# Optimization experiments

Measured on AMD Instinct MI355X. Metric: run time of the kernel, lower is better.

## Reference

```python
import jax, jax.numpy as jnp
import numpy as np

THRESHOLD = 0.2
MARGIN = 2
TEMP = 0.1


def _margin_mask(h0, w0, h1, w1):
    # interior-valid mask per spatial dim (margin_remove=b removed on both ends;
    # mask0 is None so h0s=h0 etc. and the symmetric trailing-b removal applies)
    def interior(n):
        i = jnp.arange(n)
        return (i >= MARGIN) & (i < n - MARGIN)
    m = (interior(h0)[:, None, None, None]
         & interior(w0)[None, :, None, None]
         & interior(h1)[None, None, :, None]
         & interior(w1)[None, None, None, :])  # [h0,w0,h1,w1]
    return m.reshape(1, h0 * w0, h1 * w1)


def setup_inputs() -> dict:
    key = jax.random.key(0)
    k0, k1 = jax.random.split(key)
    x0 = jax.random.normal(k0, (1, 6400, 256), dtype=jnp.float32)
    x1 = jax.random.normal(k1, (1, 6400, 256), dtype=jnp.float32)
    return {"x0": x0, "x1": x1, "h0": 80, "w0": 80, "h1": 80, "w1": 80}


def reference(x0, x1, h0, w0, h1, w1):
    n, l, c = x0.shape
    s = x1.shape[1]
    # similarities = einsum / c / temp
    sim = jnp.einsum('nlc,nsc->nls', x0, x1) / (c * TEMP)
    # dual softmax confidences
    conf = jax.nn.softmax(sim, axis=2) * jax.nn.softmax(sim, axis=1)
    # threshold + margin removal (mask0=None branch of _remove_mask_margin)
    mask = (conf > THRESHOLD) & _margin_mask(h0, w0, h1, w1)
    # mutual top-1 (argmax via equality with row/col max, exactly as torch)
    m0 = conf == jnp.max(conf, axis=2, keepdims=True)
    m1 = conf == jnp.max(conf, axis=1, keepdims=True)
    mask = mask & m0 & m1
    # fixed-shape encoding of the match extraction: nonzero(mask) <=> nonzero of
    # this masked confidence map; matched confidences are its nonzero values.
    return conf * mask.astype(conf.dtype)
```

## Files before the change

### kernel.cpp

```cpp
#include <hip/hip_runtime.h>

namespace {

constexpr int Ldim = 6400;
constexpr int Sdim = 6400;
constexpr float INV_CT = 0.0390625f;
constexpr float THR = 0.2f;
constexpr int CAP = 65536;

typedef __attribute__((ext_vector_type(8))) short short8;
typedef __attribute__((ext_vector_type(4))) float f32x4;

__device__ __forceinline__ void atomicMaxPosF(float* addr, float v) {
  atomicMax(reinterpret_cast<unsigned int*>(addr), __float_as_uint(v));
}

__device__ __forceinline__ bool valid80(int idx) {
  const int i = idx / 80;
  const int j = idx - i * 80;
  return (i >= 2) & (i < 78) & (j >= 2) & (j < 78);
}

__device__ __forceinline__ unsigned short f2bf(float v) {
  unsigned u = __float_as_uint(v);
  return (unsigned short)((u + 0x7fffu + ((u >> 16) & 1u)) >> 16);
}

__device__ __forceinline__ float conf1(float s, float rs, float cs) {
  return expf(2.f * s) / (rs * cs);
}

typedef const __attribute__((address_space(1))) unsigned int guint;
typedef __attribute__((address_space(3))) unsigned int suint;
__device__ __forceinline__ void gload16(const void* g, void* l) {
  __builtin_amdgcn_global_load_lds((guint*)g, (suint*)l, 16, 0, 0);
}


__global__ __launch_bounds__(256)
void k_split2(const float* __restrict__ X0, const float* __restrict__ X1,
              unsigned short* __restrict__ XA, unsigned short* __restrict__ XB,
              float* __restrict__ stats ) {
  const int half = Ldim * 32 / 256;
  if (blockIdx.x == 2 * half) {
    for (int i = threadIdx.x; i < 4 * Ldim + 4; i += 256) stats[i] = 0.f;
    return;
  }
  const bool second = blockIdx.x >= half;
  const float* X = second ? X1 : X0;
  unsigned short* Xh = second ? XB : XA;
  const int g = (blockIdx.x - (second ? half : 0)) * 256 + threadIdx.x;
  const int r = g >> 5;
  const int gt = g & 31;
  const float* src = X + ((size_t)r << 8) + (gt << 3);
  const float4 a = *reinterpret_cast<const float4*>(src);
  const float4 b = *reinterpret_cast<const float4*>(src + 4);
  short8 hv;
  hv[0] = (short)f2bf(a.x); hv[1] = (short)f2bf(a.y);
  hv[2] = (short)f2bf(a.z); hv[3] = (short)f2bf(a.w);
  hv[4] = (short)f2bf(b.x); hv[5] = (short)f2bf(b.y);
  hv[6] = (short)f2bf(b.z); hv[7] = (short)f2bf(b.w);
  const int gp = (gt & 3) ^ ((r >> 1) & 3);
  const size_t dst = ((size_t)((gt >> 2) * Ldim + r) * 4 + gp) << 3;
  *reinterpret_cast<short8*>(Xh + dst) = hv;
}

__device__ __forceinline__ void gemm128(
    const unsigned short* __restrict__ A, const unsigned short* __restrict__ B,
    int m0, int n0, int wave, int lane,
    unsigned short (*sA)[4096], unsigned short (*sB)[4096], f32x4 acc[4][4]) {
  const int wr = wave >> 1, wc = wave & 1;
  const int ll = lane & 15;
  const int lg = lane >> 4;
  const int arow = lane >> 2;
  const int gsel = (lane & 3) * 8;

#pragma unroll
  for (int mi = 0; mi < 4; ++mi)
#pragma unroll
    for (int ni = 0; ni < 4; ++ni) acc[mi][ni] = (f32x4){0.f, 0.f, 0.f, 0.f};

  auto stage = [&](int slot, int ks) {
    const size_t kb = (size_t)ks * (Ldim * 32);
#pragma unroll
    for (int p = 0; p < 2; ++p) {
      const int ch = wave * 2 + p;
      const size_t asrc = kb + (size_t)(m0 + ch * 16 + arow) * 32 + gsel;
      const size_t bsrc = kb + (size_t)(n0 + ch * 16 + arow) * 32 + gsel;
      gload16(A + asrc, &sA[slot][ch * 512]);
      gload16(B + bsrc, &sB[slot][ch * 512]);
    }
  };

  stage(0, 0);
  __syncthreads();

  for (int ks = 0; ks < 8; ++ks) {
    const int cur = ks & 1;
    if (ks < 7) stage(cur ^ 1, ks + 1);

    auto rd = [&](unsigned short* S, int row) -> short8 {
      const int gp = lg ^ ((row >> 1) & 3);
      return *reinterpret_cast<const short8*>(&S[(row * 4 + gp) * 8]);
    };
    short8 af[4], bfv[4];
#pragma unroll
    for (int mi = 0; mi < 4; ++mi) af[mi] = rd(sA[cur], wr * 64 + mi * 16 + ll);
#pragma unroll
    for (int ni = 0; ni < 4; ++ni) bfv[ni] = rd(sB[cur], wc * 64 + ni * 16 + ll);
#pragma unroll
    for (int mi = 0; mi < 4; ++mi)
#pragma unroll
      for (int ni = 0; ni < 4; ++ni)
        acc[mi][ni] = __builtin_amdgcn_mfma_f32_16x16x32_bf16(af[mi], bfv[ni], acc[mi][ni], 0, 0, 0);

    __syncthreads();
  }

#pragma unroll
  for (int mi = 0; mi < 4; ++mi)
#pragma unroll
    for (int ni = 0; ni < 4; ++ni) acc[mi][ni] *= INV_CT;
}

__global__ __launch_bounds__(256)
void k_gemm_all(const unsigned short* __restrict__ A, const unsigned short* __restrict__ B,
                float* __restrict__ Rsum, float* __restrict__ Csum,
                unsigned int* __restrict__ cnt, unsigned int* __restrict__ cidx,
                float* __restrict__ csim, float* __restrict__ out) {
  __shared__ unsigned short sA[2][4096], sB[2][4096];
  const int tid = threadIdx.x;
  const int lane = tid & 63, wave = tid >> 6;
  const int wr = wave >> 1, wc = wave & 1;
  const int ll = lane & 15, lg = lane >> 4;
  const int bx = blockIdx.x % (Sdim / 128);
  const int by = blockIdx.x / (Sdim / 128);
  const int m0 = by * 128, n0 = bx * 128;

  f32x4 acc[4][4];
  gemm128(A, B, m0, n0, wave, lane, sA, sB, acc);

  {
    const float4 z = make_float4(0.f, 0.f, 0.f, 0.f);
#pragma unroll
    for (int i = 0; i < 16; ++i) {
      const int e = i * 256 + tid;
      const int row = e >> 5;
      const int c4 = e & 31;
      *reinterpret_cast<float4*>(&out[(size_t)(m0 + row) * Sdim + n0 + c4 * 4]) = z;
    }
  }

  float re[16];
  float colp[4] = {0.f, 0.f, 0.f, 0.f};
#pragma unroll
  for (int mi = 0; mi < 4; ++mi)
#pragma unroll
    for (int r = 0; r < 4; ++r) {
      float s = 0.f;
#pragma unroll
      for (int ni = 0; ni < 4; ++ni) {
        const float e = expf(acc[mi][ni][r]);
        s += e;
        colp[ni] += e;
      }
      s += __shfl_xor(s, 1);
      s += __shfl_xor(s, 2);
      s += __shfl_xor(s, 4);
      s += __shfl_xor(s, 8);
      re[mi * 4 + r] = s;
      if (ll == 0)
        atomicAdd(&Rsum[m0 + wr * 64 + mi * 16 + lg * 4 + r], s);
    }
  float clw[4];
#pragma unroll
  for (int ni = 0; ni < 4; ++ni) {
    float c = colp[ni];
    c += __shfl_xor(c, 16);
    c += __shfl_xor(c, 32);
    clw[ni] = c;
    if (lane < 16) atomicAdd(&Csum[n0 + wc * 64 + ni * 16 + lane], c);
  }

  constexpr float L018 = -1.7147984f;
  float lc[4];
#pragma unroll
  for (int ni = 0; ni < 4; ++ni) lc[ni] = 0.5f * logf(clw[ni]);
#pragma unroll
  for (int mi = 0; mi < 4; ++mi)
#pragma unroll
    for (int r = 0; r < 4; ++r) {
      const float tr = 0.5f * (L018 + logf(re[mi * 4 + r]));
#pragma unroll
      for (int ni = 0; ni < 4; ++ni) {
        if (acc[mi][ni][r] > tr + lc[ni]) {
          const int row = m0 + wr * 64 + mi * 16 + lg * 4 + r;
          const int col = n0 + wc * 64 + ni * 16 + ll;
          const unsigned t = atomicAdd(cnt, 1u);
          if (t < CAP) {
            cidx[t] = (unsigned)row * Sdim + col;
            csim[t] = acc[mi][ni][r];
          }
        }
      }
    }
}

__global__ __launch_bounds__(256)
void k_final1(const unsigned int* __restrict__ cnt, const unsigned int* __restrict__ cidx,
              const float* __restrict__ csim, const float* __restrict__ Rsum,
              const float* __restrict__ Csum, float* __restrict__ RM,
              float* __restrict__ CM, float* __restrict__ cconf) {
  const int n = (int)min(*cnt, (unsigned)CAP);
  for (int i = blockIdx.x * 256 + threadIdx.x; i < n; i += gridDim.x * 256) {
    const unsigned idx = cidx[i];
    const int l = idx / Sdim;
    const int s = idx - l * Sdim;
    const float c = conf1(csim[i], Rsum[l], Csum[s]);
    cconf[i] = c;
    atomicMaxPosF(&RM[l], c);
    atomicMaxPosF(&CM[s], c);
  }
}

__global__ __launch_bounds__(256)
void k_final2(const unsigned int* __restrict__ cnt, const unsigned int* __restrict__ cidx,
              const float* __restrict__ cconf, const float* __restrict__ RM,
              const float* __restrict__ CM, float* __restrict__ out) {
  const int n = (int)min(*cnt, (unsigned)CAP);
  for (int i = blockIdx.x * 256 + threadIdx.x; i < n; i += gridDim.x * 256) {
    const unsigned idx = cidx[i];
    const int l = idx / Sdim;
    const int s = idx - l * Sdim;
    const float c = cconf[i];
    if (c > THR && valid80(l) && valid80(s) && c == RM[l] && c == CM[s])
      out[idx] = c;
  }
}

}

extern "C" void kernel_launch(void* const* d_in, const int* in_sizes, int n_in,
                              void* d_out, int out_size, void* d_ws, size_t ws_size,
                              hipStream_t stream) {
  (void)in_sizes; (void)n_in; (void)out_size; (void)ws_size;
  const float* x0 = reinterpret_cast<const float*>(d_in[0]);
  const float* x1 = reinterpret_cast<const float*>(d_in[1]);
  float* out = reinterpret_cast<float*>(d_out);

  float* Rsum = reinterpret_cast<float*>(d_ws);
  float* Csum = Rsum + Ldim;
  float* RM = Csum + Sdim;
  float* CM = RM + Ldim;
  unsigned int* cnt = reinterpret_cast<unsigned int*>(CM + Sdim);
  unsigned int* cidx = cnt + 4;
  float* csim = reinterpret_cast<float*>(cidx + CAP);
  float* cconf = csim + CAP;
  unsigned short* XA = reinterpret_cast<unsigned short*>(cconf + CAP);
  const size_t PSZ = (size_t)8 * Ldim * 32;
  unsigned short* XB = XA + PSZ;

  k_split2<<<2 * (Ldim * 32 / 256) + 1, 256, 0, stream>>>(x0, x1, XA, XB, Rsum);
  k_gemm_all<<<(Ldim / 128) * (Sdim / 128), 256, 0, stream>>>(
      XA, XB, Rsum, Csum, cnt, cidx, csim, out);
  k_final1<<<32, 256, 0, stream>>>(cnt, cidx, csim, Rsum, Csum, RM, CM, cconf);
  k_final2<<<32, 256, 0, stream>>>(cnt, cidx, cconf, RM, CM, out);
}
```

Baseline: 260.0 us.

## Stage full K dimension into LDS upfront and overlap output zeroing with loads

The double-buffered K loop is replaced by issuing all eight K-slices of A and B into LDS at once, with eight slots per operand instead of two. The zeroing of the output tile now runs while the later B slices are still in flight. Compute on slices 0–1 starts before a single mid-point barrier, and the remaining slices follow without per-step barriers. This removes the per-iteration synchronisation and load/compute serialisation, but raises LDS use to about 128KB per block, which likely allows only one block per CU and reduces latency hiding in the heavy softmax/atomic epilogue.

```diff
diff --git a/kernel.cpp b/kernel.cpp
--- a/kernel.cpp
+++ b/kernel.cpp
@@ -65,81 +65,41 @@
   *reinterpret_cast<short8*>(Xh + dst) = hv;
 }
 
-__device__ __forceinline__ void gemm128(
-    const unsigned short* __restrict__ A, const unsigned short* __restrict__ B,
-    int m0, int n0, int wave, int lane,
-    unsigned short (*sA)[4096], unsigned short (*sB)[4096], f32x4 acc[4][4]) {
-  const int wr = wave >> 1, wc = wave & 1;
-  const int ll = lane & 15;
-  const int lg = lane >> 4;
-  const int arow = lane >> 2;
-  const int gsel = (lane & 3) * 8;
-
-#pragma unroll
-  for (int mi = 0; mi < 4; ++mi)
-#pragma unroll
-    for (int ni = 0; ni < 4; ++ni) acc[mi][ni] = (f32x4){0.f, 0.f, 0.f, 0.f};
-
-  auto stage = [&](int slot, int ks) {
-    const size_t kb = (size_t)ks * (Ldim * 32);
-#pragma unroll
-    for (int p = 0; p < 2; ++p) {
-      const int ch = wave * 2 + p;
-      const size_t asrc = kb + (size_t)(m0 + ch * 16 + arow) * 32 + gsel;
-      const size_t bsrc = kb + (size_t)(n0 + ch * 16 + arow) * 32 + gsel;
-      gload16(A + asrc, &sA[slot][ch * 512]);
-      gload16(B + bsrc, &sB[slot][ch * 512]);
-    }
-  };
-
-  stage(0, 0);
-  __syncthreads();
-
-  for (int ks = 0; ks < 8; ++ks) {
-    const int cur = ks & 1;
-    if (ks < 7) stage(cur ^ 1, ks + 1);
-
-    auto rd = [&](unsigned short* S, int row) -> short8 {
-      const int gp = lg ^ ((row >> 1) & 3);
-      return *reinterpret_cast<const short8*>(&S[(row * 4 + gp) * 8]);
-    };
-    short8 af[4], bfv[4];
-#pragma unroll
-    for (int mi = 0; mi < 4; ++mi) af[mi] = rd(sA[cur], wr * 64 + mi * 16 + ll);
-#pragma unroll
-    for (int ni = 0; ni < 4; ++ni) bfv[ni] = rd(sB[cur], wc * 64 + ni * 16 + ll);
-#pragma unroll
-    for (int mi = 0; mi < 4; ++mi)
-#pragma unroll
-      for (int ni = 0; ni < 4; ++ni)
-        acc[mi][ni] = __builtin_amdgcn_mfma_f32_16x16x32_bf16(af[mi], bfv[ni], acc[mi][ni], 0, 0, 0);
-
-    __syncthreads();
-  }
-
-#pragma unroll
-  for (int mi = 0; mi < 4; ++mi)
-#pragma unroll
-    for (int ni = 0; ni < 4; ++ni) acc[mi][ni] *= INV_CT;
-}
-
 __global__ __launch_bounds__(256)
 void k_gemm_all(const unsigned short* __restrict__ A, const unsigned short* __restrict__ B,
                 float* __restrict__ Rsum, float* __restrict__ Csum,
                 unsigned int* __restrict__ cnt, unsigned int* __restrict__ cidx,
                 float* __restrict__ csim, float* __restrict__ out) {
-  __shared__ unsigned short sA[2][4096], sB[2][4096];
+  __shared__ unsigned short sA[8][4096], sB[8][4096];
   const int tid = threadIdx.x;
   const int lane = tid & 63, wave = tid >> 6;
   const int wr = wave >> 1, wc = wave & 1;
   const int ll = lane & 15, lg = lane >> 4;
+  const int arow = lane >> 2;
+  const int gsel = (lane & 3) * 8;
   const int bx = blockIdx.x % (Sdim / 128);
   const int by = blockIdx.x / (Sdim / 128);
   const int m0 = by * 128, n0 = bx * 128;
 
-  f32x4 acc[4][4];
-  gemm128(A, B, m0, n0, wave, lane, sA, sB, acc);
-
+  auto stA = [&](int ks, int p) {
+    const int ch = wave * 2 + p;
+    const size_t src = (size_t)ks * (Ldim * 32) + (size_t)(m0 + ch * 16 + arow) * 32 + gsel;
+    gload16(A + src, &sA[ks][ch * 512]);
+  };
+  auto stB = [&](int ks, int p) {
+    const int ch = wave * 2 + p;
+    const size_t src = (size_t)ks * (Ldim * 32) + (size_t)(n0 + ch * 16 + arow) * 32 + gsel;
+    gload16(B + src, &sB[ks][ch * 512]);
+  };
+
+#pragma unroll
+  for (int ks = 0; ks < 8; ++ks) { stA(ks, 0); stA(ks, 1); }
+#pragma unroll
+  for (int ks = 0; ks < 2; ++ks) { stB(ks, 0); stB(ks, 1); }
+  __syncthreads();
+
+#pragma unroll
+  for (int ks = 2; ks < 8; ++ks) { stB(ks, 0); stB(ks, 1); }
   {
     const float4 z = make_float4(0.f, 0.f, 0.f, 0.f);
 #pragma unroll
@@ -150,6 +110,40 @@
       *reinterpret_cast<float4*>(&out[(size_t)(m0 + row) * Sdim + n0 + c4 * 4]) = z;
     }
   }
+
+  f32x4 acc[4][4];
+#pragma unroll
+  for (int mi = 0; mi < 4; ++mi)
+#pragma unroll
+    for (int ni = 0; ni < 4; ++ni) acc[mi][ni] = (f32x4){0.f, 0.f, 0.f, 0.f};
+
+  auto rd = [&](const unsigned short (*S)[4096], int ks, int row) -> short8 {
+    const int gp = lg ^ ((row >> 1) & 3);
+    return *reinterpret_cast<const short8*>(&S[ks][(row * 4 + gp) * 8]);
+  };
+  auto compute_ks = [&](int ks) {
+    short8 af[4], bfv[4];
+#pragma unroll
+    for (int mi = 0; mi < 4; ++mi) af[mi] = rd(sA, ks, wr * 64 + mi * 16 + ll);
+#pragma unroll
+    for (int ni = 0; ni < 4; ++ni) bfv[ni] = rd(sB, ks, wc * 64 + ni * 16 + ll);
+#pragma unroll
+    for (int mi = 0; mi < 4; ++mi)
+#pragma unroll
+      for (int ni = 0; ni < 4; ++ni)
+        acc[mi][ni] = __builtin_amdgcn_mfma_f32_16x16x32_bf16(af[mi], bfv[ni], acc[mi][ni], 0, 0, 0);
+  };
+
+  compute_ks(0);
+  compute_ks(1);
+  __syncthreads();
+#pragma unroll
+  for (int ks = 2; ks < 8; ++ks) compute_ks(ks);
+
+#pragma unroll
+  for (int mi = 0; mi < 4; ++mi)
+#pragma unroll
+    for (int ni = 0; ni < 4; ++ni) acc[mi][ni] *= INV_CT;
 
   float re[16];
   float colp[4] = {0.f, 0.f, 0.f, 0.f};
```

Measured after the change: 289.0 us. +11.2%, slower.
